# Optimization experiments

Measured on AMD Instinct MI355X. Metric: run time of the kernel, lower is better.

## Reference

```python
import jax, jax.numpy as jnp
import numpy as np

MASK_VAL = -50000.0
HEADS = 16


def setup_inputs() -> dict:
    key = jax.random.key(0)
    ks = jax.random.split(key, 6)
    b, n, m, d = 2, 2048, 1024, 1024
    s = 0.02  # xavier-ish init scale
    x = jax.random.normal(ks[0], (b, n, d), jnp.float32)
    context = jax.random.normal(ks[1], (b, m, d), jnp.float32)
    mask = jnp.ones((b, n), dtype=bool)
    context_mask = jnp.ones((b, m), dtype=bool)
    Wq = jax.random.normal(ks[2], (d, d), jnp.float32) * s
    bq = jnp.zeros((d,), jnp.float32)
    Wkv = jax.random.normal(ks[3], (d, 2 * d), jnp.float32) * s
    bkv = jnp.zeros((2 * d,), jnp.float32)
    Wo = jax.random.normal(ks[4], (d, d), jnp.float32) * s
    bo = jnp.zeros((d,), jnp.float32)
    return {"x": x, "context": context, "Wq": Wq, "bq": bq, "Wkv": Wkv,
            "bkv": bkv, "Wo": Wo, "bo": bo, "mask": mask,
            "context_mask": context_mask}


def reference(x, context, Wq, bq, Wkv, bkv, Wo, bo, mask, context_mask):
    b, n, d = x.shape
    m = context.shape[1]
    h = HEADS
    dh = d // h
    scale = dh ** -0.5

    kv_input = jnp.concatenate([x, context], axis=1)  # [b, n+m, d]
    q = (x @ Wq + bq).reshape(b, n, h, dh).transpose(0, 2, 1, 3)  # [b,h,n,dh]
    kv = kv_input @ Wkv + bkv
    k, v = jnp.split(kv, 2, axis=-1)
    k = k.reshape(b, n + m, h, dh).transpose(0, 2, 1, 3)  # [b,h,n+m,dh]
    v = v.reshape(b, n + m, h, dh).transpose(0, 2, 1, 3)

    dots = jnp.einsum('bhid,bhjd->bhij', q * scale, k)  # [b,h,n,n+m]

    # padding mask: self block uses q_mask x q_mask, cross block q_mask x k_mask
    self_mask = mask[:, None, :, None] & mask[:, None, None, :]          # [b,1,n,n]
    cross_mask = mask[:, None, :, None] & context_mask[:, None, None, :]  # [b,1,n,m]
    input_mask = jnp.concatenate([self_mask, cross_mask], axis=-1)
    dots = jnp.where(input_mask, dots, MASK_VAL)

    # causal masking applies only to the first n (self) key columns,
    # matching torch's dots[:, :, triu_i, triu_j] = MASK_VAL with i,j < n
    causal = jnp.triu(jnp.ones((n, n), dtype=bool), 1)
    causal = jnp.concatenate([causal, jnp.zeros((n, m), dtype=bool)], axis=1)
    dots = jnp.where(causal[None, None], MASK_VAL, dots)

    attn = jax.nn.softmax(dots, axis=-1)  # dropout omitted (eval mode)
    out = jnp.einsum('bhij,bhjd->bhid', attn, v)
    out = out.transpose(0, 2, 1, 3).reshape(b, n, d)
    return out @ Wo + bo
```

## Files before the change

### kernel.cpp

```cpp
#include <hip/hip_runtime.h>

typedef __bf16 bf16;
typedef bf16 bf16x2 __attribute__((ext_vector_type(2)));
typedef bf16 bf16x4 __attribute__((ext_vector_type(4)));
typedef bf16 bf16x8 __attribute__((ext_vector_type(8)));
typedef float floatx4 __attribute__((ext_vector_type(4)));
typedef float floatx16 __attribute__((ext_vector_type(16)));
typedef unsigned int uintx4 __attribute__((ext_vector_type(4)));

__device__ __forceinline__ floatx4 mfma16(bf16x8 a, bf16x8 b, floatx4 c) {
  return __builtin_amdgcn_mfma_f32_16x16x32_bf16(a, b, c, 0, 0, 0);
}
__device__ __forceinline__ floatx16 mfma32(bf16x8 a, bf16x8 b, floatx16 c) {
  return __builtin_amdgcn_mfma_f32_32x32x16_bf16(a, b, c, 0, 0, 0);
}

__device__ __forceinline__ void async_ld16(const bf16* g, bf16* lds) {
  __builtin_amdgcn_global_load_lds(
      (const __attribute__((address_space(1))) void*)g,
      (__attribute__((address_space(3))) void*)lds, 16, 0, 0);
}

__global__ __launch_bounds__(256) void prep(
    const float* __restrict__ x, const float* __restrict__ ctx,
    const float* __restrict__ Wq, const float* __restrict__ Wkv,
    const float* __restrict__ Wo, bf16* __restrict__ kvin,
    bf16* __restrict__ WT, bf16* __restrict__ WoT) {
  __shared__ float tile[32][33];
  int bid = blockIdx.x;
  if (bid < 6144) {
    int idx = bid * 256 + threadIdx.x;
    int row = idx >> 8;
    int c4 = (idx & 255) << 2;
    int b = row / 3072, l = row - b * 3072;
    const float* src = (l < 2048)
        ? (x + ((size_t)b * 2048 + l) * 1024 + c4)
        : (ctx + ((size_t)b * 1024 + (l - 2048)) * 1024 + c4);
    float4 v = *(const float4*)src;
    bf16x4 o = { (bf16)v.x, (bf16)v.y, (bf16)v.z, (bf16)v.w };
    *(bf16x4*)(kvin + (size_t)row * 1024 + c4) = o;
    return;
  }
  const float* W; bf16* OT; int N, t;
  if (bid < 7168)      { W = Wq;  OT = WT;                        N = 1024; t = bid - 6144; }
  else if (bid < 9216) { W = Wkv; OT = WT + (size_t)1024 * 1024;  N = 2048; t = bid - 7168; }
  else                 { W = Wo;  OT = WoT;                       N = 1024; t = bid - 9216; }
  int nb = N >> 5;
  int n0 = (t % nb) * 32, k0 = (t / nb) * 32;
  int tx = threadIdx.x & 31, ty = threadIdx.x >> 5;
  for (int i = 0; i < 4; i++) {
    int kk = ty + i * 8;
    tile[kk][tx] = W[(size_t)(k0 + kk) * N + n0 + tx];
  }
  __syncthreads();
  for (int i = 0; i < 4; i++) {
    int nn = ty + i * 8;
    OT[(size_t)(n0 + nn) * 1024 + k0 + tx] = (bf16)tile[tx][nn];
  }
}

__global__ __launch_bounds__(512, 4) void gemm_qkv(
    const bf16* __restrict__ A, const bf16* __restrict__ Bt,
    const float* __restrict__ bq, const float* __restrict__ bkv,
    bf16* __restrict__ Qb, bf16* __restrict__ Kb, bf16* __restrict__ Vt) {
  int id = blockIdx.x;
  int col0, row0;
  if (id < 384) {
    col0 = 1024 + ((id & 15) << 7);
    row0 = (id >> 4) << 8;
  } else {
    int q = id - 384;
    col0 = (q & 7) << 7;
    int rb = q >> 3;
    row0 = (rb < 8 ? rb : rb + 4) << 8;
  }
  __shared__ bf16 As[256 * 64];
  __shared__ bf16 Bs[128 * 64];
  int tid = threadIdx.x;
  int wave = tid >> 6, lane = tid & 63;
  int lane15 = lane & 15, quad = lane >> 4;
  int wm = (wave & 3) * 64, wn = (wave >> 2) * 64;
  int sr = tid >> 3;
  int ssl = ((tid & 7) ^ (sr & 7)) * 8;
  floatx4 acc[4][4] = {};
  for (int k0 = 0; k0 < 1024; k0 += 64) {
    for (int p = 0; p < 4; p++)
      async_ld16(A + (size_t)(row0 + p * 64 + sr) * 1024 + k0 + ssl,
                 &As[p * 4096 + tid * 8]);
    for (int p = 0; p < 2; p++)
      async_ld16(Bt + (size_t)(col0 + p * 64 + sr) * 1024 + k0 + ssl,
                 &Bs[p * 4096 + tid * 8]);
    __syncthreads();
    for (int kh = 0; kh < 2; kh++) {
      bf16x8 af[4], bfr[4];
      for (int t = 0; t < 4; t++) {
        int row = wm + t * 16 + lane15;
        af[t] = *(const bf16x8*)(
            &As[row * 64 + (((kh << 2) | quad) ^ (row & 7)) * 8]);
      }
      for (int t = 0; t < 4; t++) {
        int row = wn + t * 16 + lane15;
        bfr[t] = *(const bf16x8*)(
            &Bs[row * 64 + (((kh << 2) | quad) ^ (row & 7)) * 8]);
      }
      for (int tm = 0; tm < 4; tm++)
        for (int tn = 0; tn < 4; tn++)
          acc[tm][tn] = mfma16(af[tm], bfr[tn], acc[tm][tn]);
    }
    __syncthreads();
  }
  float bv[4];
  for (int tn = 0; tn < 4; tn++) {
    int col = col0 + wn + tn * 16 + lane15;
    bv[tn] = (col < 1024) ? bq[col] : bkv[col - 1024];
  }
  int bb = row0 / 3072;
  int l0 = row0 - bb * 3072;
  if (col0 < 1024) {
    const float SQ = 0.18033688011f;
    for (int tm = 0; tm < 4; tm++)
      for (int r = 0; r < 4; r++) {
        size_t grow = (size_t)bb * 2048 + l0 + wm + tm * 16 + quad * 4 + r;
        for (int tn = 0; tn < 4; tn++)
          Qb[grow * 1024 + col0 + wn + tn * 16 + lane15] =
              (bf16)((acc[tm][tn][r] + bv[tn]) * SQ);
      }
  } else if (col0 < 2048) {
    for (int tm = 0; tm < 4; tm++)
      for (int r = 0; r < 4; r++) {
        size_t grow = row0 + wm + tm * 16 + quad * 4 + r;
        for (int tn = 0; tn < 4; tn++)
          Kb[grow * 1024 + (col0 - 1024) + wn + tn * 16 + lane15] =
              (bf16)(acc[tm][tn][r] + bv[tn]);
      }
  } else {
    for (int tm = 0; tm < 4; tm++) {
      int lr = l0 + wm + tm * 16 + quad * 4;
      for (int tn = 0; tn < 4; tn++) {
        int c = col0 - 2048 + wn + tn * 16 + lane15;
        bf16x4 pk = { (bf16)(acc[tm][tn][0] + bv[tn]),
                      (bf16)(acc[tm][tn][1] + bv[tn]),
                      (bf16)(acc[tm][tn][2] + bv[tn]),
                      (bf16)(acc[tm][tn][3] + bv[tn]) };
        *(bf16x4*)(Vt + ((size_t)bb * 1024 + c) * 3072 + lr) = pk;
      }
    }
  }
}

__global__ __launch_bounds__(256) void gemm_o(
    const bf16* __restrict__ A, const bf16* __restrict__ Bt,
    const float* __restrict__ bias, float* __restrict__ O) {
  int col0 = blockIdx.x * 64, row0 = blockIdx.y * 128;
  __shared__ bf16 As[128 * 128];
  __shared__ bf16 Bs[64 * 128];
  int tid = threadIdx.x;
  int wave = tid >> 6, lane = tid & 63;
  int lane15 = lane & 15, quad = lane >> 4;
  int wm = (wave & 1) * 64, wn = (wave >> 1) * 32;
  int sr = tid >> 4;
  int ssl = ((tid & 15) ^ (sr & 7)) * 8;
  floatx4 acc[4][2] = {};
  for (int k0 = 0; k0 < 1024; k0 += 128) {
    for (int p = 0; p < 8; p++)
      async_ld16(A + (size_t)(row0 + p * 16 + sr) * 1024 + k0 + ssl,
                 &As[p * 2048 + tid * 8]);
    for (int p = 0; p < 4; p++)
      async_ld16(Bt + (size_t)(col0 + p * 16 + sr) * 1024 + k0 + ssl,
                 &Bs[p * 2048 + tid * 8]);
    __syncthreads();
    for (int kh = 0; kh < 4; kh++) {
      bf16x8 af[4], bfr[2];
      for (int t = 0; t < 4; t++) {
        int row = wm + t * 16 + lane15;
        af[t] = *(const bf16x8*)(
            &As[row * 128 + (((kh << 2) | quad) ^ (row & 7)) * 8]);
      }
      for (int t = 0; t < 2; t++) {
        int row = wn + t * 16 + lane15;
        bfr[t] = *(const bf16x8*)(
            &Bs[row * 128 + (((kh << 2) | quad) ^ (row & 7)) * 8]);
      }
      for (int tm = 0; tm < 4; tm++)
        for (int tn = 0; tn < 2; tn++)
          acc[tm][tn] = mfma16(af[tm], bfr[tn], acc[tm][tn]);
    }
    __syncthreads();
  }
  float bv[2];
  for (int tn = 0; tn < 2; tn++)
    bv[tn] = bias[col0 + wn + tn * 16 + lane15];
  for (int tm = 0; tm < 4; tm++)
    for (int r = 0; r < 4; r++) {
      size_t grow = row0 + wm + tm * 16 + quad * 4 + r;
      for (int tn = 0; tn < 2; tn++)
        O[grow * 1024 + col0 + wn + tn * 16 + lane15] = acc[tm][tn][r] + bv[tn];
    }
}

__global__ __launch_bounds__(256, 4) void flash_attn(
    const bf16* __restrict__ Qb, const bf16* __restrict__ Kb,
    const bf16* __restrict__ Vt, bf16* __restrict__ Ob) {
  const int LD = 72;
  __shared__ bf16 Ks[2][64 * LD];
  __shared__ bf16 Vs[2][64 * LD];
  int tid = threadIdx.x;
  int wave = tid >> 6, lane = tid & 63;
  int qsub = wave & 1, grp = wave >> 1;
  int l31 = lane & 31, half = lane >> 5;
  int blk = blockIdx.x;
  int qt = 31 - (blk >> 5);
  int bh = blk & 31;
  int h = bh & 15, b = bh >> 4;
  int q0 = qt * 64;
  int qw0 = q0 + qsub * 32;
  int qq = qw0 + l31;

  const bf16* qrow = Qb + ((size_t)(b * 2048 + qq)) * 1024 + h * 64 + half * 8;
  bf16x8 qf[4];
  for (int c = 0; c < 4; c++) qf[c] = *(const bf16x8*)(qrow + c * 16);

  floatx16 Oacc[2] = {};
  float l_part = 0.f;

  int nself = qt + 1;
  int T = nself + 16;
  int iters = (T + 1 - grp) >> 1;
  int max_iters = (T + 1) >> 1;
  const bf16* kbase = Kb + (size_t)(b * 3072) * 1024 + h * 64;
  const bf16* vbase = Vt + ((size_t)b * 1024 + h * 64) * 3072;

  int tidg = qsub * 64 + lane;
  int sr = tidg >> 1, sc = (tidg & 1) * 32;
  bf16x8 kreg[4], vreg[4];
  auto prefetch = [&](int t) {
    int keyrow = (t < nself) ? t * 64 : 2048 + (t - nself) * 64;
    const bf16* kp = kbase + (size_t)(keyrow + sr) * 1024 + sc;
    const bf16* vp = vbase + (size_t)sr * 3072 + keyrow + sc;
    for (int j = 0; j < 4; j++) {
      kreg[j] = *(const bf16x8*)(kp + j * 8);
      vreg[j] = *(const bf16x8*)(vp + j * 8);
    }
  };
  int t = grp;
  prefetch(t);

  bf16* ksg = &Ks[grp][0];
  bf16* vsg = &Vs[grp][0];
  for (int it = 0; it < max_iters; it++) {
    bool act = it < iters;
    int keyrow = 0;
    if (act) keyrow = (t < nself) ? t * 64 : 2048 + (t - nself) * 64;
    __syncthreads();
    if (act)
      for (int j = 0; j < 4; j++) {
        *(bf16x8*)(&ksg[sr * LD + sc + j * 8]) = kreg[j];
        *(bf16x8*)(&vsg[sr * LD + sc + j * 8]) = vreg[j];
      }
    __syncthreads();
    if (act && t + 2 < T) prefetch(t + 2);
    if (act) {
      bool is_self = t < nself;
      uintx4 pf[4];
      for (int kt = 0; kt < 2; kt++) {
        floatx16 st = {};
        const bf16* ka = &ksg[(kt * 32 + l31) * LD + half * 8];
        __builtin_amdgcn_s_setprio(1);
        for (int c = 0; c < 4; c++)
          st = mfma32(*(const bf16x8*)(ka + c * 16), qf[c], st);
        __builtin_amdgcn_s_setprio(0);
        bool need_mask = is_self && (keyrow + kt * 32 + 31 > qw0);
        float p[16];
        for (int r = 0; r < 16; r++) {
          float e = __builtin_amdgcn_exp2f(st[r]);
          if (need_mask) {
            int key = keyrow + kt * 32 + (r & 3) + 8 * (r >> 2) + half * 4;
            if (key > qq) e = 0.f;
          }
          p[r] = e;
          l_part += e;
        }
        unsigned pk[8];
        for (int m2 = 0; m2 < 8; m2++) {
          bf16x2 two = { (bf16)p[2 * m2], (bf16)p[2 * m2 + 1] };
          pk[m2] = __builtin_bit_cast(unsigned, two);
        }
        for (int c2 = 0; c2 < 2; c2++) {
          auto s02 = __builtin_amdgcn_permlane32_swap(
              pk[4 * c2 + 0], pk[4 * c2 + 2], false, false);
          auto s13 = __builtin_amdgcn_permlane32_swap(
              pk[4 * c2 + 1], pk[4 * c2 + 3], false, false);
          int c = kt * 2 + c2;
          pf[c][0] = s02[0];
          pf[c][1] = s13[0];
          pf[c][2] = s02[1];
          pf[c][3] = s13[1];
        }
      }
      __builtin_amdgcn_s_setprio(1);
      for (int vt = 0; vt < 2; vt++) {
        const bf16* va = &vsg[(vt * 32 + l31) * LD + half * 8];
        for (int c = 0; c < 4; c++)
          Oacc[vt] = mfma32(__builtin_bit_cast(bf16x8, pf[c]),
                            *(const bf16x8*)(va + c * 16), Oacc[vt]);
      }
      __builtin_amdgcn_s_setprio(0);
    }
    t += 2;
  }
  float l_tot = l_part + __shfl_xor(l_part, 32, 64);
  __syncthreads();
  float* Mb = (float*)&Ks[0][0];
  float* Lg = Mb + 4096;
  if (grp == 1) {
    for (int vt = 0; vt < 2; vt++)
      for (int r = 0; r < 16; r++)
        Mb[((qsub * 2 + vt) * 16 + r) * 64 + lane] = Oacc[vt][r];
    if (half == 0) Lg[(2 + qsub) * 32 + l31] = l_tot;
  } else if (half == 0) {
    Lg[qsub * 32 + l31] = l_tot;
  }
  __syncthreads();
  if (grp == 0) {
    for (int r = 0; r < 16; r++) {
      int qr = (r & 3) + 8 * (r >> 2) + half * 4;
      float inv = 1.0f / (Lg[qsub * 32 + qr] + Lg[(2 + qsub) * 32 + qr]);
      for (int vt = 0; vt < 2; vt++) {
        float o = Oacc[vt][r] + Mb[((qsub * 2 + vt) * 16 + r) * 64 + lane];
        Ob[(size_t)(b * 2048 + qw0 + qr) * 1024 + h * 64 + vt * 32 + l31] =
            (bf16)(o * inv);
      }
    }
  }
}

extern "C" void kernel_launch(void* const* d_in, const int* in_sizes, int n_in,
                              void* d_out, int out_size, void* d_ws,
                              size_t ws_size, hipStream_t stream) {
  const float* x   = (const float*)d_in[0];
  const float* ctx = (const float*)d_in[1];
  const float* Wq  = (const float*)d_in[2];
  const float* bq  = (const float*)d_in[3];
  const float* Wkv = (const float*)d_in[4];
  const float* bkv = (const float*)d_in[5];
  const float* Wo  = (const float*)d_in[6];
  const float* bo  = (const float*)d_in[7];
  float* out = (float*)d_out;

  bf16* p = (bf16*)d_ws;
  bf16* kvin = p;   p += (size_t)6144 * 1024;
  bf16* WT   = p;   p += (size_t)3072 * 1024;
  bf16* WoT  = p;   p += (size_t)1024 * 1024;
  bf16* Qb   = p;   p += (size_t)4096 * 1024;
  bf16* Kb   = p;   p += (size_t)6144 * 1024;
  bf16* Vt   = p;   p += (size_t)2 * 1024 * 3072;
  bf16* Ob   = p;

  prep<<<10240, 256, 0, stream>>>(x, ctx, Wq, Wkv, Wo, kvin, WT, WoT);
  gemm_qkv<<<512, 512, 0, stream>>>(kvin, WT, bq, bkv, Qb, Kb, Vt);
  flash_attn<<<1024, 256, 0, stream>>>(Qb, Kb, Vt, Ob);
  gemm_o<<<dim3(16, 32), 256, 0, stream>>>(Ob, WoT, bo, out);
}
```

Baseline: 221.0 us.

## Triple-buffer QKV GEMM shared-memory tiles with async prefetch two stages ahead

Replaces the single-buffered load-sync-compute loop in the QKV projection GEMM with a three-slot LDS ring buffer. Global-to-LDS async loads for step t+2 are issued in pieces interleaved with the MFMA work of step t, and explicit vmcnt waits replace full syncthreads. This aims to hide global memory latency behind compute. In exchange, LDS use triples to about 144KB per block, which limits occupancy, and correctness now depends on hand-counted vmcnt values.

```diff
diff --git a/kernel.cpp b/kernel.cpp
--- a/kernel.cpp
+++ b/kernel.cpp
@@ -74,40 +74,73 @@
     int rb = q >> 3;
     row0 = (rb < 8 ? rb : rb + 4) << 8;
   }
-  __shared__ bf16 As[256 * 64];
-  __shared__ bf16 Bs[128 * 64];
+  __shared__ bf16 As[3][256 * 64];
+  __shared__ bf16 Bs[3][128 * 64];
   int tid = threadIdx.x;
   int wave = tid >> 6, lane = tid & 63;
   int lane15 = lane & 15, quad = lane >> 4;
   int wm = (wave & 3) * 64, wn = (wave >> 2) * 64;
   int sr = tid >> 3;
   int ssl = ((tid & 7) ^ (sr & 7)) * 8;
-  floatx4 acc[4][4] = {};
-  for (int k0 = 0; k0 < 1024; k0 += 64) {
-    for (int p = 0; p < 4; p++)
+
+  auto stageA01 = [&](int slot, int k0) {
+    for (int p = 0; p < 2; p++)
       async_ld16(A + (size_t)(row0 + p * 64 + sr) * 1024 + k0 + ssl,
-                 &As[p * 4096 + tid * 8]);
+                 &As[slot][p * 4096 + tid * 8]);
+  };
+  auto stageA23 = [&](int slot, int k0) {
+    for (int p = 2; p < 4; p++)
+      async_ld16(A + (size_t)(row0 + p * 64 + sr) * 1024 + k0 + ssl,
+                 &As[slot][p * 4096 + tid * 8]);
+  };
+  auto stageB = [&](int slot, int k0) {
     for (int p = 0; p < 2; p++)
       async_ld16(Bt + (size_t)(col0 + p * 64 + sr) * 1024 + k0 + ssl,
-                 &Bs[p * 4096 + tid * 8]);
-    __syncthreads();
+                 &Bs[slot][p * 4096 + tid * 8]);
+  };
+  stageA01(0, 0);  stageA23(0, 0);  stageB(0, 0);
+  stageA01(1, 64); stageA23(1, 64); stageB(1, 64);
+
+  floatx4 acc[4][4] = {};
+  for (int t = 0; t < 16; t++) {
+    int cur = t % 3;
+    int nxt = (t + 2) % 3;
+    int k2 = (t + 2) << 6;
+    bool more = (t + 2) < 16;
+    if (more) stageA01(nxt, k2);
+    if (t < 14)
+      asm volatile("s_waitcnt vmcnt(8)" ::: "memory");
+    else if (t == 14)
+      asm volatile("s_waitcnt vmcnt(6)" ::: "memory");
+    else
+      asm volatile("s_waitcnt vmcnt(0)" ::: "memory");
+    __builtin_amdgcn_s_barrier();
+    const bf16* as = &As[cur][0];
+    const bf16* bs = &Bs[cur][0];
     for (int kh = 0; kh < 2; kh++) {
-      bf16x8 af[4], bfr[4];
-      for (int t = 0; t < 4; t++) {
-        int row = wm + t * 16 + lane15;
-        af[t] = *(const bf16x8*)(
-            &As[row * 64 + (((kh << 2) | quad) ^ (row & 7)) * 8]);
-      }
-      for (int t = 0; t < 4; t++) {
-        int row = wn + t * 16 + lane15;
-        bfr[t] = *(const bf16x8*)(
-            &Bs[row * 64 + (((kh << 2) | quad) ^ (row & 7)) * 8]);
-      }
-      for (int tm = 0; tm < 4; tm++)
-        for (int tn = 0; tn < 4; tn++)
-          acc[tm][tn] = mfma16(af[tm], bfr[tn], acc[tm][tn]);
-    }
-    __syncthreads();
+      bf16x8 af[4];
+      for (int tt = 0; tt < 4; tt++) {
+        int row = wm + tt * 16 + lane15;
+        af[tt] = *(const bf16x8*)(
+            &as[row * 64 + (((kh << 2) | quad) ^ (row & 7)) * 8]);
+      }
+      for (int nh = 0; nh < 2; nh++) {
+        bf16x8 bfr[2];
+        for (int tt = 0; tt < 2; tt++) {
+          int row = wn + (nh * 2 + tt) * 16 + lane15;
+          bfr[tt] = *(const bf16x8*)(
+              &bs[row * 64 + (((kh << 2) | quad) ^ (row & 7)) * 8]);
+        }
+        for (int tm = 0; tm < 4; tm++)
+          for (int tn = 0; tn < 2; tn++)
+            acc[tm][nh * 2 + tn] = mfma16(af[tm], bfr[tn], acc[tm][nh * 2 + tn]);
+        if (more) {
+          if (kh == 0 && nh == 0) stageA23(nxt, k2);
+          else if (kh == 0 && nh == 1) stageB(nxt, k2);
+        }
+      }
+    }
+    __builtin_amdgcn_s_barrier();
   }
   float bv[4];
   for (int tn = 0; tn < 4; tn++) {
```

Measured after the change: 225.8 us. +2.2%, slower.
